# Kernel tuning notes

Hardware: AMD Instinct MI355X
Metric: run time of the kernel (lower is better)

## Reference

```python
import jax, jax.numpy as jnp
import numpy as np

RADIUS = 4
SIGMA_X = 4.0
SIGMA_I = 10.0
P = 64                      # patch_size
NS = 2 * RADIUS + 1         # neighborhood_size = 9
EPS = float(np.finfo(np.float64).eps)


def _dist_weights():
    # Faithful to torch: dist varies only along the LAST window axis
    # (torch `expand` of a 1-D tensor to (9,9,9) broadcasts along dim -1).
    d = jnp.arange(1, NS + 1) - (RADIUS + 1)          # -4..4
    dist3d = jnp.broadcast_to(3 * d ** 2, (NS, NS, NS)).astype(jnp.float32)
    mask = (dist3d <= RADIUS).astype(jnp.float32)
    return (mask * jnp.exp(-dist3d / SIGMA_X ** 2)).reshape(-1)  # (729,)


_OFFSETS = jnp.asarray(
    np.stack(np.meshgrid(np.arange(NS), np.arange(NS), np.arange(NS), indexing='ij'),
             axis=-1).reshape(-1, 3), dtype=jnp.int32)            # (729, 3)


def _forward(batch, preds):
    B = batch.shape[0]
    K = preds.shape[1]
    pad = [(0, 0), (0, 0), (RADIUS, RADIUS), (RADIUS, RADIUS), (RADIUS, RADIUS)]
    pb = jnp.pad(batch, pad, constant_values=EPS)   # [B,1,P+2r,P+2r,P+2r]
    pp = jnp.pad(preds, pad, constant_values=EPS)   # [B,K,P+2r,P+2r,P+2r]
    dw = _dist_weights()

    def body(carry, od):
        off, w_o = od
        num, den = carry
        img_win = jax.lax.dynamic_slice(pb, (0, 0, off[0], off[1], off[2]),
                                        (B, 1, P, P, P))
        # Gaussian intensity affinity * spatial weight for this offset
        w = jnp.exp(-(img_win - batch) ** 2 / SIGMA_I ** 2) * w_o   # [B,1,P,P,P]
        pred_win = jax.lax.dynamic_slice(pp, (0, 0, off[0], off[1], off[2]),
                                         (B, K, P, P, P))
        return (num + w * pred_win, den + w), None

    num0 = jnp.zeros((B, K, P, P, P), batch.dtype)
    den0 = jnp.zeros((B, 1, P, P, P), batch.dtype)
    (num_map, den_map), _ = jax.lax.scan(body, (num0, den0), (_OFFSETS, dw))

    # Faithful to torch broadcasting: preds[B,1,P,P,P] * map[B,P,P,P] -> [B,B,...],
    # i.e. each sample's preds are contracted with the batch-summed maps.
    num_s = num_map.sum(axis=0)          # [K,P,P,P]
    den_s = den_map.sum(axis=0)[0]       # [P,P,P]
    numerator = jnp.einsum('bkxyz,kxyz->bk', preds, num_s)
    denominator = jnp.einsum('bkxyz,xyz->bk', preds, den_s)
    loss = (numerator + EPS) / (denominator + EPS)   # [B,K]
    return K - loss.sum(axis=1)                      # [B]


def setup_inputs() -> dict:
    key = jax.random.key(0)
    k1, k2 = jax.random.split(key)
    batch = jax.random.uniform(k1, (4, 1, P, P, P), dtype=jnp.float32)
    preds = jax.random.uniform(k2, (4, 4, P, P, P), dtype=jnp.float32)
    return {"batch": batch, "preds": preds}


def reference(batch, preds):
    return _forward(batch, preds)
```

## Files before the change

### kernel.cpp

```cpp
#include <hip/hip_runtime.h>
#include <hip/hip_fp16.h>


constexpr int Pdim = 64;
constexpr int P3   = Pdim * Pdim * Pdim;
constexpr int NREP = 16;

#define EPSF 2.2204460492503131e-16f

constexpr float WZ1   = 0.8290291181804004f;
constexpr float K2F   = 0.014426950408889634f;
constexpr float C1F   = 0.02f;
constexpr float WFULL = 81.0f * (1.0f + 2.0f * WZ1);

template<int X0, int NX, int FIRSTW>
__device__ __forceinline__ void passx_body(const float* __restrict__ Ip,
                                           const float* __restrict__ Pp,
                                           __half2* __restrict__ Uo,
                                           bool isden) {
  float w0[9], w1[9];
#pragma unroll
  for (int i = 0; i < 9; ++i) { w0[i] = 0.f; w1[i] = 0.f; }
  float s0 = 0.f, s1 = 0.f;
#pragma unroll
  for (int i = 0; i < NX; ++i) {
    const int x = X0 + i;
    float u0 = 0.f, u1 = 0.f;
    if (x < 64) {
      float I = Ip[x << 12];
      float g = exp2f(-I * I * K2F);
      float p = isden ? 1.f : Pp[x << 12];
      u0 = g * p;
      u1 = u0 * I;
    }
    const int r = i % 9;
    s0 += u0 - w0[r]; w0[r] = u0;
    s1 += u1 - w1[r]; w1[r] = u1;
    if (i >= FIRSTW) Uo[(x - 4) << 12] = __floats2half2_rn(s0, s1);
  }
}

__global__ __launch_bounds__(256)
void ncuts_passx(const float* __restrict__ batch, const float* __restrict__ preds,
                 __half2* __restrict__ U, float* __restrict__ acc) {
  const int t = threadIdx.x;
  if (blockIdx.x == 0 && blockIdx.y == 0 && blockIdx.z == 0) {
    acc[t] = 0.f; acc[t + 256] = 0.f;
  }
  const int z = t & 63, ys = t >> 6;
  const int y = blockIdx.x * 4 + ys;
  const int pair = blockIdx.y;
  const int b = pair / 5, c = pair - 5 * b;
  const bool isden = (c == 4);
  const int lin = (y << 6) + z;
  const float* Ip = batch + b * P3 + lin;
  const float* Pp = isden ? Ip : preds + (b * 4 + c) * P3 + lin;
  __half2* Uo = U + pair * P3 + lin;
  if (blockIdx.z == 0) passx_body< 0, 36, 4>(Ip, Pp, Uo, isden);
  else                 passx_body<28, 40, 8>(Ip, Pp, Uo, isden);
}

template<int Y0, int NY, int FIRSTW>
__device__ __forceinline__ void passyz_body(const __half2* __restrict__ src,
                                            __half2* __restrict__ dst, int z) {
  float w0[9], w1[9];
#pragma unroll
  for (int i = 0; i < 9; ++i) { w0[i] = 0.f; w1[i] = 0.f; }
  float s0 = 0.f, s1 = 0.f;
#pragma unroll
  for (int i = 0; i < NY; ++i) {
    const int y = Y0 + i;
    float u0 = 0.f, u1 = 0.f;
    if (y < 64) {
      float2 u = __half22float2(src[y << 6]);
      u0 = u.x; u1 = u.y;
    }
    const int r = i % 9;
    s0 += u0 - w0[r]; w0[r] = u0;
    s1 += u1 - w1[r]; w1[r] = u1;
    if (i >= FIRSTW) {
      float up0 = __shfl_up(s0, 1, 64),   up1 = __shfl_up(s1, 1, 64);
      float dn0 = __shfl_down(s0, 1, 64), dn1 = __shfl_down(s1, 1, 64);
      if (z == 0)  { up0 = 0.f; up1 = 0.f; }
      if (z == 63) { dn0 = 0.f; dn1 = 0.f; }
      float v0 = __builtin_fmaf(WZ1, up0 + dn0, s0);
      float v1 = __builtin_fmaf(WZ1, up1 + dn1, s1);
      dst[(y - 4) << 6] = __floats2half2_rn(v0, v1);
    }
  }
}

__global__ __launch_bounds__(256)
void ncuts_passyz(const __half2* __restrict__ U, __half2* __restrict__ V) {
  const int t = threadIdx.x;
  const int z = t & 63, xs = t >> 6;
  const int x = blockIdx.x * 4 + xs;
  const int pair = blockIdx.y;
  const __half2* src = U + pair * P3 + (x << 12) + z;
  __half2* dst = V + pair * P3 + (x << 12) + z;
  if (blockIdx.z == 0) passyz_body< 0, 36, 4>(src, dst, z);
  else                 passyz_body<28, 40, 8>(src, dst, z);
}

__global__ __launch_bounds__(256)
void ncuts_contract(const float* __restrict__ batch, const float* __restrict__ preds,
                    const __half2* __restrict__ V, float* __restrict__ acc) {
  __shared__ float red[4][32];
  const int t = threadIdx.x;
  float pn[16], pd[16];
#pragma unroll
  for (int i = 0; i < 16; ++i) { pn[i] = 0.f; pd[i] = 0.f; }

#pragma unroll 1
  for (int it = 0; it < 2; ++it) {
    const int v = blockIdx.x * 512 + it * 256 + t;
    const int z = v & 63, y = (v >> 6) & 63, x = v >> 12;

    float a0[4], a1[4], gsum = 0.f;
#pragma unroll
    for (int b = 0; b < 4; ++b) {
      float I = batch[b * P3 + v];
      float g = exp2f(-I * I * K2F);
      a0[b] = g; a1[b] = g * I * C1F; gsum += g;
    }

    float ns[4] = {0.f, 0.f, 0.f, 0.f};
    float ds = 0.f;
#pragma unroll
    for (int b = 0; b < 4; ++b) {
#pragma unroll
      for (int c = 0; c < 5; ++c) {
        float2 u = __half22float2(V[(b * 5 + c) * P3 + v]);
        float zc = __builtin_fmaf(a0[b], u.x, a1[b] * u.y);
        if (c < 4) ns[c] += zc;
        else       ds    += zc;
      }
    }
    float cx = (float)(9 - max(0, 4 - x) - max(0, x - 59));
    float cy = (float)(9 - max(0, 4 - y) - max(0, y - 59));
    float cz = 1.f + WZ1 * (float)((int)(z > 0) + (int)(z < 63));
    ds = __builtin_fmaf(gsum, WFULL - cx * cy * cz, ds);

#pragma unroll
    for (int b = 0; b < 4; ++b) {
#pragma unroll
      for (int k = 0; k < 4; ++k) {
        float p = preds[(b * 4 + k) * P3 + v];
        pn[b * 4 + k] = __builtin_fmaf(p, ns[k], pn[b * 4 + k]);
        pd[b * 4 + k] = __builtin_fmaf(p, ds,    pd[b * 4 + k]);
      }
    }
  }

#pragma unroll
  for (int i = 0; i < 16; ++i) {
#pragma unroll
    for (int off = 32; off > 0; off >>= 1) {
      pn[i] += __shfl_down(pn[i], off, 64);
      pd[i] += __shfl_down(pd[i], off, 64);
    }
  }
  const int wave = t >> 6, lane = t & 63;
  if (lane == 0) {
#pragma unroll
    for (int i = 0; i < 16; ++i) { red[wave][i] = pn[i]; red[wave][16 + i] = pd[i]; }
  }
  __syncthreads();
  if (t < 32) {
    float s = red[0][t] + red[1][t] + red[2][t] + red[3][t];
    atomicAdd(&acc[(blockIdx.x & (NREP - 1)) * 32 + t], s);
  }
}

__global__ void ncuts_final(const float* __restrict__ acc, float* __restrict__ out) {
  __shared__ float loss[16];
  int t = threadIdx.x;
  if (t < 16) {
    float n = 0.f, d = 0.f;
    for (int r = 0; r < NREP; ++r) { n += acc[r * 32 + t]; d += acc[r * 32 + 16 + t]; }
    loss[t] = (n + EPSF) / (d + EPSF);
  }
  __syncthreads();
  if (t < 4) {
    float s = loss[t * 4] + loss[t * 4 + 1] + loss[t * 4 + 2] + loss[t * 4 + 3];
    out[t] = 4.0f - s;
  }
}

constexpr int Rxy = 4;
constexpr int TX = 8, TY = 8;
constexpr int ZLEN = 2;
constexpr int RGX = 16, RGY = 16, RGZ = 10;
constexpr int YP = 17, ZP = 11;

__global__ __launch_bounds__(256, 2)
void ncuts_main(const float* __restrict__ batch, const float* __restrict__ preds,
                float* __restrict__ acc) {
  __shared__ float  sB[RGX][YP][ZP];
  __shared__ float4 sP[RGX][YP][ZP];
  __shared__ float  red[4][32];

  const int t = threadIdx.x;
  const int tx = t & 7, ty = (t >> 3) & 7, tzt = t >> 6;
  const int bx0 = blockIdx.x * TX, by0 = blockIdx.y * TY, bz0 = blockIdx.z * 8;
  const int x = bx0 + tx, y = by0 + ty, z0 = bz0 + tzt * ZLEN;
  const int zc = tzt * ZLEN;

  float  den[ZLEN];
  float4 num[ZLEN];
#pragma unroll
  for (int j = 0; j < ZLEN; ++j) { den[j] = 0.f; num[j] = make_float4(0.f, 0.f, 0.f, 0.f); }

  const float C1 = -0.014426950408889634f;
  const float LWZ1 = -0.27050531991668065f;

  for (int b = 0; b < 4; ++b) {
    __syncthreads();
    for (int idx = t; idx < RGX * RGY * RGZ; idx += 256) {
      int rz = idx % RGZ, rq = idx / RGZ, ry = rq % RGY, rx = rq / RGY;
      int gx = bx0 + rx - Rxy, gy = by0 + ry - Rxy, gz = bz0 + rz - 1;
      bool in = ((unsigned)gx < 64u) & ((unsigned)gy < 64u) & ((unsigned)gz < 64u);
      float v = EPSF; float4 pv = make_float4(EPSF, EPSF, EPSF, EPSF);
      if (in) {
        int gi = (gx * Pdim + gy) * Pdim + gz;
        v = batch[b * P3 + gi];
        const float* pp = preds + b * 4 * P3 + gi;
        pv.x = pp[0]; pv.y = pp[P3]; pv.z = pp[2 * P3]; pv.w = pp[3 * P3];
      }
      sB[rx][ry][rz] = v; sP[rx][ry][rz] = pv;
    }
    __syncthreads();

    float I0[ZLEN];
#pragma unroll
    for (int j = 0; j < ZLEN; ++j) I0[j] = sB[tx + Rxy][ty + Rxy][zc + 1 + j];

#pragma unroll 1
    for (int dy = 0; dy < 9; ++dy) {
#pragma unroll 3
      for (int dx = 0; dx < 9; ++dx) {
        const float*  cb = &sB[tx + dx][ty + dy][zc];
        const float4* cp = &sP[tx + dx][ty + dy][zc];
        float colB[ZLEN + 2]; float4 colP[ZLEN + 2];
#pragma unroll
        for (int j = 0; j < ZLEN + 2; ++j) { colB[j] = cb[j]; colP[j] = cp[j]; }
#pragma unroll
        for (int j = 0; j < ZLEN; ++j) {
#pragma unroll
          for (int dz = 0; dz < 3; ++dz) {
            float d = colB[j + dz] - I0[j];
            float arg = __builtin_fmaf(d * d, C1, (dz == 1) ? 0.f : LWZ1);
            float w = exp2f(arg);
            den[j] += w;
            float4 p = colP[j + dz];
            num[j].x = __builtin_fmaf(w, p.x, num[j].x);
            num[j].y = __builtin_fmaf(w, p.y, num[j].y);
            num[j].z = __builtin_fmaf(w, p.z, num[j].z);
            num[j].w = __builtin_fmaf(w, p.w, num[j].w);
          }
        }
      }
    }
  }

  float pn[16], pd[16];
#pragma unroll
  for (int i = 0; i < 16; ++i) { pn[i] = 0.f; pd[i] = 0.f; }
#pragma unroll
  for (int b = 0; b < 4; ++b) {
#pragma unroll
    for (int j = 0; j < ZLEN; ++j) {
      const float* pp = preds + b * 4 * P3 + ((x * Pdim + y) * Pdim + z0 + j);
      float nsv[4] = {num[j].x, num[j].y, num[j].z, num[j].w};
#pragma unroll
      for (int k = 0; k < 4; ++k) {
        float pv = pp[k * P3];
        pn[b * 4 + k] = __builtin_fmaf(pv, nsv[k], pn[b * 4 + k]);
        pd[b * 4 + k] = __builtin_fmaf(pv, den[j], pd[b * 4 + k]);
      }
    }
  }
#pragma unroll
  for (int i = 0; i < 16; ++i) {
#pragma unroll
    for (int off = 32; off > 0; off >>= 1) {
      pn[i] += __shfl_down(pn[i], off, 64);
      pd[i] += __shfl_down(pd[i], off, 64);
    }
  }
  const int wave = t >> 6, lane = t & 63;
  if (lane == 0) {
#pragma unroll
    for (int i = 0; i < 16; ++i) { red[wave][i] = pn[i]; red[wave][16 + i] = pd[i]; }
  }
  __syncthreads();
  if (t < 32) {
    float s = red[0][t] + red[1][t] + red[2][t] + red[3][t];
    int bid = blockIdx.x + 8 * (blockIdx.y + 8 * (int)blockIdx.z);
    atomicAdd(&acc[(bid & (NREP - 1)) * 32 + t], s);
  }
}

__global__ void ncuts_zero(float* __restrict__ acc) {
  int t = threadIdx.x;
  if (t < NREP * 32) acc[t] = 0.f;
}

extern "C" void kernel_launch(void* const* d_in, const int* in_sizes, int n_in,
                              void* d_out, int out_size, void* d_ws, size_t ws_size,
                              hipStream_t stream) {
  const float* batch = (const float*)d_in[0];
  const float* preds = (const float*)d_in[1];
  float* out = (float*)d_out;

  const size_t fbytes = (size_t)20 * P3 * sizeof(__half2);
  const size_t need   = 2 * fbytes + 8192;
  if (ws_size >= need) {
    __half2* U   = (__half2*)((char*)d_ws + 256);
    __half2* V   = (__half2*)((char*)d_ws + 256 + fbytes);
    float*   acc = (float*)((char*)d_ws + 512 + 2 * fbytes);
    hipLaunchKernelGGL(ncuts_passx,  dim3(16, 20, 2), dim3(256), 0, stream,
                       batch, preds, U, acc);
    hipLaunchKernelGGL(ncuts_passyz, dim3(16, 20, 2), dim3(256), 0, stream, U, V);
    hipLaunchKernelGGL(ncuts_contract, dim3(512), dim3(256), 0, stream,
                       batch, preds, V, acc);
    hipLaunchKernelGGL(ncuts_final, dim3(1), dim3(64), 0, stream, acc, out);
  } else {
    float* acc = (float*)d_ws;
    hipLaunchKernelGGL(ncuts_zero, dim3(1), dim3(512), 0, stream, acc);
    hipLaunchKernelGGL(ncuts_main, dim3(8, 8, 8), dim3(256), 0, stream,
                       batch, preds, acc);
    hipLaunchKernelGGL(ncuts_final, dim3(1), dim3(64), 0, stream, acc, out);
  }
}
```

Before: 97.08 us.

## Share gaussian across channels in x pass, cache affinity, fuse final reduction

The x-pass now has one thread handle all five channels of a batch sample, so the intensity load and exp are computed once instead of five times. The same pass also writes a half-precision affinity buffer A that the contract kernel reads instead of recomputing exp from batch. The x and y passes switch to four 16-wide chunks with a 4-element halo each, and the contract kernel processes two voxels per thread using vectorized loads. The separate final kernel is replaced by a last-block ticket inside contract, which removes one launch but adds more register pressure and an extra buffer write.

```diff
diff --git a/kernel.cpp b/kernel.cpp
--- a/kernel.cpp
+++ b/kernel.cpp
@@ -13,72 +13,92 @@
 constexpr float C1F   = 0.02f;
 constexpr float WFULL = 81.0f * (1.0f + 2.0f * WZ1);
 
-template<int X0, int NX, int FIRSTW>
-__device__ __forceinline__ void passx_body(const float* __restrict__ Ip,
-                                           const float* __restrict__ Pp,
-                                           __half2* __restrict__ Uo,
-                                           bool isden) {
+__global__ __launch_bounds__(128)
+void ncuts_passx(const float* __restrict__ batch, const float* __restrict__ preds,
+                 __half2* __restrict__ U, __half2* __restrict__ A,
+                 float* __restrict__ acc, unsigned* __restrict__ ticket) {
+  const int t = threadIdx.x;
+  if (blockIdx.x == 0 && blockIdx.y == 0 && blockIdx.z == 0) {
+    acc[t * 4 + 0] = 0.f; acc[t * 4 + 1] = 0.f;
+    acc[t * 4 + 2] = 0.f; acc[t * 4 + 3] = 0.f;
+    if (t == 0) *ticket = 0u;
+  }
+  const int z = t & 63, yh = t >> 6;
+  const int y = blockIdx.x * 2 + yh;
+  const int b = blockIdx.y;
+  const int X0 = 16 * (int)blockIdx.z - 4;
+  const int lin = (y << 6) + z;
+  const float* Ip = batch + b * P3 + lin;
+  const float* Pp = preds + b * 4 * P3 + lin;
+  __half2* Ub = U + (b * 5) * P3 + lin;
+  __half2* Ab = A + b * P3 + lin;
+
+  float w[10][9], sum[10];
+#pragma unroll
+  for (int f = 0; f < 10; ++f) {
+    sum[f] = 0.f;
+#pragma unroll
+    for (int i = 0; i < 9; ++i) w[f][i] = 0.f;
+  }
+
+#pragma unroll
+  for (int i = 0; i < 24; ++i) {
+    const int x = X0 + i;
+    float u[10];
+    if ((unsigned)x < 64u) {
+      float I = Ip[x << 12];
+      float g = exp2f(-I * I * K2F);
+#pragma unroll
+      for (int c = 0; c < 4; ++c) {
+        float p = Pp[c * P3 + (x << 12)];
+        u[2 * c]     = g * p;
+        u[2 * c + 1] = u[2 * c] * I;
+      }
+      u[8] = g; u[9] = g * I;
+      if (i >= 4 && i < 20)
+        Ab[x << 12] = __floats2half2_rn(g, g * I * C1F);
+    } else {
+#pragma unroll
+      for (int f = 0; f < 10; ++f) u[f] = 0.f;
+    }
+    const int r = i % 9;
+#pragma unroll
+    for (int f = 0; f < 10; ++f) { sum[f] += u[f] - w[f][r]; w[f][r] = u[f]; }
+    if (i >= 8) {
+      const int xo = x - 4;
+#pragma unroll
+      for (int c = 0; c < 5; ++c)
+        Ub[c * P3 + (xo << 12)] = __floats2half2_rn(sum[2 * c], sum[2 * c + 1]);
+    }
+  }
+}
+
+__global__ __launch_bounds__(256)
+void ncuts_passyz(const __half2* __restrict__ U, __half2* __restrict__ V) {
+  const int t = threadIdx.x;
+  const int z = t & 63, xh = t >> 6;
+  const int x = blockIdx.x * 4 + xh;
+  const int pair = blockIdx.y;
+  const int Y0 = 16 * (int)blockIdx.z - 4;
+  const __half2* src = U + pair * P3 + (x << 12) + z;
+  __half2* dst = V + pair * P3 + (x << 12) + z;
+
   float w0[9], w1[9];
 #pragma unroll
   for (int i = 0; i < 9; ++i) { w0[i] = 0.f; w1[i] = 0.f; }
   float s0 = 0.f, s1 = 0.f;
 #pragma unroll
-  for (int i = 0; i < NX; ++i) {
-    const int x = X0 + i;
+  for (int i = 0; i < 24; ++i) {
+    const int y = Y0 + i;
     float u0 = 0.f, u1 = 0.f;
-    if (x < 64) {
-      float I = Ip[x << 12];
-      float g = exp2f(-I * I * K2F);
-      float p = isden ? 1.f : Pp[x << 12];
-      u0 = g * p;
-      u1 = u0 * I;
+    if ((unsigned)y < 64u) {
+      float2 u = __half22float2(src[y << 6]);
+      u0 = u.x; u1 = u.y;
     }
     const int r = i % 9;
     s0 += u0 - w0[r]; w0[r] = u0;
     s1 += u1 - w1[r]; w1[r] = u1;
-    if (i >= FIRSTW) Uo[(x - 4) << 12] = __floats2half2_rn(s0, s1);
-  }
-}
-
-__global__ __launch_bounds__(256)
-void ncuts_passx(const float* __restrict__ batch, const float* __restrict__ preds,
-                 __half2* __restrict__ U, float* __restrict__ acc) {
-  const int t = threadIdx.x;
-  if (blockIdx.x == 0 && blockIdx.y == 0 && blockIdx.z == 0) {
-    acc[t] = 0.f; acc[t + 256] = 0.f;
-  }
-  const int z = t & 63, ys = t >> 6;
-  const int y = blockIdx.x * 4 + ys;
-  const int pair = blockIdx.y;
-  const int b = pair / 5, c = pair - 5 * b;
-  const bool isden = (c == 4);
-  const int lin = (y << 6) + z;
-  const float* Ip = batch + b * P3 + lin;
-  const float* Pp = isden ? Ip : preds + (b * 4 + c) * P3 + lin;
-  __half2* Uo = U + pair * P3 + lin;
-  if (blockIdx.z == 0) passx_body< 0, 36, 4>(Ip, Pp, Uo, isden);
-  else                 passx_body<28, 40, 8>(Ip, Pp, Uo, isden);
-}
-
-template<int Y0, int NY, int FIRSTW>
-__device__ __forceinline__ void passyz_body(const __half2* __restrict__ src,
-                                            __half2* __restrict__ dst, int z) {
-  float w0[9], w1[9];
-#pragma unroll
-  for (int i = 0; i < 9; ++i) { w0[i] = 0.f; w1[i] = 0.f; }
-  float s0 = 0.f, s1 = 0.f;
-#pragma unroll
-  for (int i = 0; i < NY; ++i) {
-    const int y = Y0 + i;
-    float u0 = 0.f, u1 = 0.f;
-    if (y < 64) {
-      float2 u = __half22float2(src[y << 6]);
-      u0 = u.x; u1 = u.y;
-    }
-    const int r = i % 9;
-    s0 += u0 - w0[r]; w0[r] = u0;
-    s1 += u1 - w1[r]; w1[r] = u1;
-    if (i >= FIRSTW) {
+    if (i >= 8) {
       float up0 = __shfl_up(s0, 1, 64),   up1 = __shfl_up(s1, 1, 64);
       float dn0 = __shfl_down(s0, 1, 64), dn1 = __shfl_down(s1, 1, 64);
       if (z == 0)  { up0 = 0.f; up1 = 0.f; }
@@ -91,64 +111,57 @@
 }
 
 __global__ __launch_bounds__(256)
-void ncuts_passyz(const __half2* __restrict__ U, __half2* __restrict__ V) {
-  const int t = threadIdx.x;
-  const int z = t & 63, xs = t >> 6;
-  const int x = blockIdx.x * 4 + xs;
-  const int pair = blockIdx.y;
-  const __half2* src = U + pair * P3 + (x << 12) + z;
-  __half2* dst = V + pair * P3 + (x << 12) + z;
-  if (blockIdx.z == 0) passyz_body< 0, 36, 4>(src, dst, z);
-  else                 passyz_body<28, 40, 8>(src, dst, z);
-}
-
-__global__ __launch_bounds__(256)
-void ncuts_contract(const float* __restrict__ batch, const float* __restrict__ preds,
-                    const __half2* __restrict__ V, float* __restrict__ acc) {
+void ncuts_contract(const float* __restrict__ preds, const __half2* __restrict__ A,
+                    const __half2* __restrict__ V, float* __restrict__ acc,
+                    unsigned* __restrict__ ticket, float* __restrict__ out) {
   __shared__ float red[4][32];
-  const int t = threadIdx.x;
+  __shared__ int islast;
+  const int t   = threadIdx.x;
+  const int idx = blockIdx.x * 256 + t;
+  const int v0  = idx << 1;
+  const int z = v0 & 63, y = (v0 >> 6) & 63, x = v0 >> 12;
+
+  float a0[4][2], a1[4][2], gsum[2] = {0.f, 0.f};
+#pragma unroll
+  for (int b = 0; b < 4; ++b) {
+    float2 raw = *(const float2*)(A + b * P3 + v0);
+    float2 f0 = __half22float2(__builtin_bit_cast(__half2, raw.x));
+    float2 f1 = __half22float2(__builtin_bit_cast(__half2, raw.y));
+    a0[b][0] = f0.x; a1[b][0] = f0.y;
+    a0[b][1] = f1.x; a1[b][1] = f1.y;
+    gsum[0] += f0.x; gsum[1] += f1.x;
+  }
+
+  float ns[4][2] = {{0.f,0.f},{0.f,0.f},{0.f,0.f},{0.f,0.f}};
+  float ds[2] = {0.f, 0.f};
+#pragma unroll
+  for (int b = 0; b < 4; ++b) {
+#pragma unroll
+    for (int c = 0; c < 5; ++c) {
+      float2 raw = *(const float2*)(V + (b * 5 + c) * P3 + v0);
+      float2 u0 = __half22float2(__builtin_bit_cast(__half2, raw.x));
+      float2 u1 = __half22float2(__builtin_bit_cast(__half2, raw.y));
+      float zc0 = __builtin_fmaf(a0[b][0], u0.x, a1[b][0] * u0.y);
+      float zc1 = __builtin_fmaf(a0[b][1], u1.x, a1[b][1] * u1.y);
+      if (c < 4) { ns[c][0] += zc0; ns[c][1] += zc1; }
+      else       { ds[0]    += zc0; ds[1]    += zc1; }
+    }
+  }
+  float cx = 9.f - (float)max(0, 4 - x) - (float)max(0, x - 59);
+  float cy = 9.f - (float)max(0, 4 - y) - (float)max(0, y - 59);
+  float cz0 = 1.f + WZ1 * ((z > 0 ? 1.f : 0.f) + 1.f);
+  float cz1 = 1.f + WZ1 * (1.f + (z + 1 < 63 ? 1.f : 0.f));
+  ds[0] = __builtin_fmaf(gsum[0], WFULL - cx * cy * cz0, ds[0]);
+  ds[1] = __builtin_fmaf(gsum[1], WFULL - cx * cy * cz1, ds[1]);
+
   float pn[16], pd[16];
 #pragma unroll
-  for (int i = 0; i < 16; ++i) { pn[i] = 0.f; pd[i] = 0.f; }
-
-#pragma unroll 1
-  for (int it = 0; it < 2; ++it) {
-    const int v = blockIdx.x * 512 + it * 256 + t;
-    const int z = v & 63, y = (v >> 6) & 63, x = v >> 12;
-
-    float a0[4], a1[4], gsum = 0.f;
-#pragma unroll
-    for (int b = 0; b < 4; ++b) {
-      float I = batch[b * P3 + v];
-      float g = exp2f(-I * I * K2F);
-      a0[b] = g; a1[b] = g * I * C1F; gsum += g;
-    }
-
-    float ns[4] = {0.f, 0.f, 0.f, 0.f};
-    float ds = 0.f;
-#pragma unroll
-    for (int b = 0; b < 4; ++b) {
-#pragma unroll
-      for (int c = 0; c < 5; ++c) {
-        float2 u = __half22float2(V[(b * 5 + c) * P3 + v]);
-        float zc = __builtin_fmaf(a0[b], u.x, a1[b] * u.y);
-        if (c < 4) ns[c] += zc;
-        else       ds    += zc;
-      }
-    }
-    float cx = (float)(9 - max(0, 4 - x) - max(0, x - 59));
-    float cy = (float)(9 - max(0, 4 - y) - max(0, y - 59));
-    float cz = 1.f + WZ1 * (float)((int)(z > 0) + (int)(z < 63));
-    ds = __builtin_fmaf(gsum, WFULL - cx * cy * cz, ds);
-
-#pragma unroll
-    for (int b = 0; b < 4; ++b) {
-#pragma unroll
-      for (int k = 0; k < 4; ++k) {
-        float p = preds[(b * 4 + k) * P3 + v];
-        pn[b * 4 + k] = __builtin_fmaf(p, ns[k], pn[b * 4 + k]);
-        pd[b * 4 + k] = __builtin_fmaf(p, ds,    pd[b * 4 + k]);
-      }
+  for (int b = 0; b < 4; ++b) {
+#pragma unroll
+    for (int k = 0; k < 4; ++k) {
+      float2 p = *(const float2*)(preds + (b * 4 + k) * P3 + v0);
+      pn[b * 4 + k] = p.x * ns[k][0] + p.y * ns[k][1];
+      pd[b * 4 + k] = p.x * ds[0]    + p.y * ds[1];
     }
   }
 
@@ -170,39 +183,44 @@
     float s = red[0][t] + red[1][t] + red[2][t] + red[3][t];
     atomicAdd(&acc[(blockIdx.x & (NREP - 1)) * 32 + t], s);
   }
-}
-
-__global__ void ncuts_final(const float* __restrict__ acc, float* __restrict__ out) {
-  __shared__ float loss[16];
-  int t = threadIdx.x;
-  if (t < 16) {
-    float n = 0.f, d = 0.f;
-    for (int r = 0; r < NREP; ++r) { n += acc[r * 32 + t]; d += acc[r * 32 + 16 + t]; }
-    loss[t] = (n + EPSF) / (d + EPSF);
-  }
-  __syncthreads();
-  if (t < 4) {
-    float s = loss[t * 4] + loss[t * 4 + 1] + loss[t * 4 + 2] + loss[t * 4 + 3];
-    out[t] = 4.0f - s;
+  __syncthreads();
+  if (t == 0) {
+    unsigned done = atomicAdd(ticket, 1u);
+    islast = (done == gridDim.x - 1);
+  }
+  __syncthreads();
+  if (islast) {
+    if (t < 32) {
+      float n = 0.f;
+      for (int r = 0; r < NREP; ++r) n += atomicAdd(&acc[r * 32 + t], 0.f);
+      red[0][t] = n;
+    }
+    __syncthreads();
+    if (t < 4) {
+      float s = 0.f;
+      for (int k = 0; k < 4; ++k)
+        s += (red[0][t * 4 + k] + EPSF) / (red[0][16 + t * 4 + k] + EPSF);
+      out[t] = 4.0f - s;
+    }
   }
 }
 
 constexpr int Rxy = 4;
-constexpr int TX = 8, TY = 8;
+constexpr int TXf = 8, TYf = 8;
 constexpr int ZLEN = 2;
 constexpr int RGX = 16, RGY = 16, RGZ = 10;
-constexpr int YP = 17, ZP = 11;
+constexpr int YPf = 17, ZPf = 11;
 
 __global__ __launch_bounds__(256, 2)
-void ncuts_main(const float* __restrict__ batch, const float* __restrict__ preds,
-                float* __restrict__ acc) {
-  __shared__ float  sB[RGX][YP][ZP];
-  __shared__ float4 sP[RGX][YP][ZP];
+void ncuts_mainf(const float* __restrict__ batch, const float* __restrict__ preds,
+                 float* __restrict__ acc) {
+  __shared__ float  sB[RGX][YPf][ZPf];
+  __shared__ float4 sP[RGX][YPf][ZPf];
   __shared__ float  red[4][32];
 
   const int t = threadIdx.x;
   const int tx = t & 7, ty = (t >> 3) & 7, tzt = t >> 6;
-  const int bx0 = blockIdx.x * TX, by0 = blockIdx.y * TY, bz0 = blockIdx.z * 8;
+  const int bx0 = blockIdx.x * TXf, by0 = blockIdx.y * TYf, bz0 = blockIdx.z * 8;
   const int x = bx0 + tx, y = by0 + ty, z0 = bz0 + tzt * ZLEN;
   const int zc = tzt * ZLEN;
 
@@ -306,6 +324,21 @@
   if (t < NREP * 32) acc[t] = 0.f;
 }
 
+__global__ void ncuts_final(const float* __restrict__ acc, float* __restrict__ out) {
+  __shared__ float loss[16];
+  int t = threadIdx.x;
+  if (t < 16) {
+    float n = 0.f, d = 0.f;
+    for (int r = 0; r < NREP; ++r) { n += acc[r * 32 + t]; d += acc[r * 32 + 16 + t]; }
+    loss[t] = (n + EPSF) / (d + EPSF);
+  }
+  __syncthreads();
+  if (t < 4) {
+    float s = loss[t * 4] + loss[t * 4 + 1] + loss[t * 4 + 2] + loss[t * 4 + 3];
+    out[t] = 4.0f - s;
+  }
+}
+
 extern "C" void kernel_launch(void* const* d_in, const int* in_sizes, int n_in,
                               void* d_out, int out_size, void* d_ws, size_t ws_size,
                               hipStream_t stream) {
@@ -313,22 +346,26 @@
   const float* preds = (const float*)d_in[1];
   float* out = (float*)d_out;
 
-  const size_t fbytes = (size_t)20 * P3 * sizeof(__half2);
-  const size_t need   = 2 * fbytes + 8192;
+  const size_t ub = (size_t)20 * P3 * sizeof(__half2);
+  const size_t vb = ub;
+  const size_t ab = (size_t)4 * P3 * sizeof(__half2);
+  const size_t need = ub + vb + ab + 8192;
   if (ws_size >= need) {
-    __half2* U   = (__half2*)((char*)d_ws + 256);
-    __half2* V   = (__half2*)((char*)d_ws + 256 + fbytes);
-    float*   acc = (float*)((char*)d_ws + 512 + 2 * fbytes);
-    hipLaunchKernelGGL(ncuts_passx,  dim3(16, 20, 2), dim3(256), 0, stream,
-                       batch, preds, U, acc);
-    hipLaunchKernelGGL(ncuts_passyz, dim3(16, 20, 2), dim3(256), 0, stream, U, V);
+    char* base = (char*)d_ws;
+    __half2*  U      = (__half2*)(base + 256);
+    __half2*  V      = (__half2*)(base + 256 + ub);
+    __half2*  A      = (__half2*)(base + 256 + ub + vb);
+    float*    acc    = (float*)(base + 512 + ub + vb + ab);
+    unsigned* ticket = (unsigned*)(base + 512 + ub + vb + ab + 2048);
+    hipLaunchKernelGGL(ncuts_passx, dim3(32, 4, 4), dim3(128), 0, stream,
+                       batch, preds, U, A, acc, ticket);
+    hipLaunchKernelGGL(ncuts_passyz, dim3(16, 20, 4), dim3(256), 0, stream, U, V);
     hipLaunchKernelGGL(ncuts_contract, dim3(512), dim3(256), 0, stream,
-                       batch, preds, V, acc);
-    hipLaunchKernelGGL(ncuts_final, dim3(1), dim3(64), 0, stream, acc, out);
+                       preds, A, V, acc, ticket, out);
   } else {
     float* acc = (float*)d_ws;
     hipLaunchKernelGGL(ncuts_zero, dim3(1), dim3(512), 0, stream, acc);
-    hipLaunchKernelGGL(ncuts_main, dim3(8, 8, 8), dim3(256), 0, stream,
+    hipLaunchKernelGGL(ncuts_mainf, dim3(8, 8, 8), dim3(256), 0, stream,
                        batch, preds, acc);
     hipLaunchKernelGGL(ncuts_final, dim3(1), dim3(64), 0, stream, acc, out);
   }
```

Measured after the change: 102.7 us. +5.8%, slower.
